# Kernel tuning notes

Hardware: AMD Instinct MI355X
Metric: run time of the kernel (lower is better)

## Reference

```python
import jax, jax.numpy as jnp
import numpy as np

N = 1024       # sentence length (words incl. root at index 0)
WD = 300       # word embedding dim (GloVe-style)
PD = 25        # pos_emb_dim
H = 125        # hidden_dim_lstm
FC = 100       # hidden_dim_fc
PVOCAB = 50    # POS tagset size


def setup_inputs() -> dict:
    key = jax.random.key(0)
    ks = jax.random.split(key, 14)
    f = lambda k, s: jax.random.normal(k, s, dtype=jnp.float32) * 0.1
    d_in = WD + PD
    return {
        "word_vecs": jax.random.normal(ks[0], (N, WD), dtype=jnp.float32),
        "pos_idx": jax.random.randint(ks[1], (N,), 0, PVOCAB),
        "parents_ids": jax.random.randint(ks[2], (N,), 0, N),
        "pos_emb": f(ks[3], (PVOCAB, PD)),
        "Wih0": f(ks[4], (2, 4 * H, d_in)),
        "Whh0": f(ks[5], (2, 4 * H, H)),
        "b0": f(ks[6], (2, 4 * H)),
        "Wih1": f(ks[7], (2, 4 * H, 2 * H)),
        "Whh1": f(ks[8], (2, 4 * H, H)),
        "b1": f(ks[9], (2, 4 * H)),
        "fc1_W": f(ks[10], (FC, 4 * H)),
        "fc1_b": f(ks[11], (FC,)),
        "fc2_W": f(ks[12], (1, FC)),
        "fc2_b": f(ks[13], (1,)),
    }


def _lstm_dir(x, Wih, Whh, b, reverse):
    # torch LSTM cell, gate order (i, f, g, o); b = b_ih + b_hh
    Hd = Whh.shape[1]
    def step(carry, xt):
        h, c = carry
        g = xt @ Wih.T + h @ Whh.T + b
        i, fg, gg, o = jnp.split(g, 4)
        i = jax.nn.sigmoid(i)
        fg = jax.nn.sigmoid(fg)
        gg = jnp.tanh(gg)
        o = jax.nn.sigmoid(o)
        c = fg * c + i * gg
        h = o * jnp.tanh(c)
        return (h, c), h
    init = (jnp.zeros((Hd,), x.dtype), jnp.zeros((Hd,), x.dtype))
    _, hs = jax.lax.scan(step, init, x, reverse=reverse)
    return hs  # [n, H], already in original time order


def _bilstm_layer(x, Wih, Whh, b):
    hf = _lstm_dir(x, Wih[0], Whh[0], b[0], False)
    hb = _lstm_dir(x, Wih[1], Whh[1], b[1], True)
    return jnp.concatenate([hf, hb], axis=1)  # [n, 2H]


def reference(word_vecs, pos_idx, parents_ids, pos_emb, Wih0, Whh0, b0,
              Wih1, Whh1, b1, fc1_W, fc1_b, fc2_W, fc2_b):
    # encoder: concat word + pos embeddings, 2-layer BiLSTM
    x = jnp.concatenate([word_vecs, pos_emb[pos_idx]], axis=1)  # [n, WD+PD]
    h = _bilstm_layer(x, Wih0, Whh0, b0)
    h = _bilstm_layer(h, Wih1, Whh1, b1)  # [n, 2H]
    n = h.shape[0]
    twoH = h.shape[1]
    # fc1(cat(h_i, h_j)) = h_i @ W_head^T + h_j @ W_child^T + b  (vectorized over all pairs)
    A = h @ fc1_W[:, :twoH].T   # head contribution  [n, FC]
    B = h @ fc1_W[:, twoH:].T   # child contribution [n, FC]
    T = jnp.tanh(A[:, None, :] + B[None, :, :] + fc1_b)  # [n, n, FC]
    raw = T @ fc2_W[0] + fc2_b[0]                         # [n, n]
    ii = jnp.arange(n)
    # original loop skips diagonal and arcs into the root (j == 0); those stay 0
    mask = (ii[:, None] != ii[None, :]) & (ii[None, :] != 0)
    scores_mat = jnp.where(mask, raw, jnp.float32(0.0))
    logits = scores_mat.T  # row j = scores of heads for child j
    logp = jax.nn.log_softmax(logits, axis=1)
    loss = -jnp.mean(logp[jnp.arange(n), parents_ids])
    return loss, scores_mat
```

## Files before the change

kernel.cpp:

```cpp
#include <hip/hip_runtime.h>

typedef float v2f __attribute__((ext_vector_type(2)));
typedef float v4f __attribute__((ext_vector_type(4)));

#define LOG2E 1.4426950408889634f
#define LN2   0.6931471805599453f

__device__ __forceinline__ float fexp2(float x) {
  float r; asm("v_exp_f32 %0, %1" : "=v"(r) : "v"(x)); return r;
}
__device__ __forceinline__ float fexp2n(float x) {
  float r; asm("v_exp_f32 %0, -%1" : "=v"(r) : "v"(x)); return r;
}
__device__ __forceinline__ float frcp(float x) {
  float r; asm("v_rcp_f32 %0, %1" : "=v"(r) : "v"(x)); return r;
}
__device__ __forceinline__ float flog2(float x) {
  float r; asm("v_log_f32 %0, %1" : "=v"(r) : "v"(x)); return r;
}
__device__ __forceinline__ void pkfma(v2f& c, v2f a, v2f b) {
  asm("v_pk_fma_f32 %0, %1, %2, %0" : "+v"(c) : "v"(a), "v"(b));
}
__device__ __forceinline__ float dpp_xor1(float v) {
  return __builtin_bit_cast(float,
      __builtin_amdgcn_update_dpp(0, __builtin_bit_cast(int, v), 0xB1, 0xF, 0xF, true));
}
__device__ __forceinline__ float dpp_xor2(float v) {
  return __builtin_bit_cast(float,
      __builtin_amdgcn_update_dpp(0, __builtin_bit_cast(int, v), 0x4E, 0xF, 0xF, true));
}
__device__ __forceinline__ void barrier_lgkm() {
  asm volatile("s_waitcnt lgkmcnt(0)\n\ts_barrier" ::: "memory");
}

__global__ void k_embed(const float* __restrict__ wv, const int* __restrict__ pidx,
                        const float* __restrict__ pemb, float* __restrict__ X) {
  int t = blockIdx.x;
  int pi = pidx[t];
  for (int c = threadIdx.x; c < 336; c += 128) {
    float v;
    if (c < 300)      v = wv[t * 300 + c];
    else if (c < 325) v = pemb[pi * 25 + (c - 300)];
    else              v = 0.f;
    X[t * 336 + c] = v;
  }
}

__global__ void k_repack(const float* __restrict__ src, float* __restrict__ dst,
                         int sK, int dK, int doScale) {
  int r = blockIdx.x;
  float sc = 1.f;
  if (doScale) { int gate = (r % 500) / 125; sc = (gate == 2) ? 0.5f * LOG2E : 0.25f * LOG2E; }
  for (int c = threadIdx.x; c < dK; c += 128)
    dst[r * dK + c] = (c < sK) ? src[r * sK + c] * sc : 0.f;
}

__global__ void k_bscale(const float* __restrict__ b, float* __restrict__ bs) {
  int i = blockIdx.x * 256 + threadIdx.x;
  if (i < 1000) {
    int gate = (i % 500) / 125;
    bs[i] = b[i] * ((gate == 2) ? 0.5f * LOG2E : 0.25f * LOG2E);
  }
}

__global__ void k_wab(const float* __restrict__ fc1W, float* __restrict__ Wab) {
  int r = blockIdx.x;
  int sr = (r < 100) ? r : r - 100;
  int so = (r < 100) ? 0 : 250;
  for (int c = threadIdx.x; c < 256; c += 128)
    Wab[r * 256 + c] = (c < 250) ? fc1W[sr * 500 + so + c] : 0.f;
}

__global__ void k_misc(const float* __restrict__ fc1b, const float* __restrict__ fc2W,
                       float* __restrict__ biasAB, float* __restrict__ sumw) {
  __shared__ float red[128];
  int t = threadIdx.x;
  for (int c = t; c < 256; c += 128)
    biasAB[c] = (c < 100) ? fc1b[c] : 0.f;
  float s = (t < 100) ? fc2W[t] : 0.f;
  red[t] = s; __syncthreads();
  for (int off = 64; off; off >>= 1) {
    if (t < off) red[t] += red[t + off];
    __syncthreads();
  }
  if (t == 0) sumw[0] = red[0];
}

#define BM 64
#define BN 64
#define BKK 16
__global__ __launch_bounds__(256) void k_gemm(
    const float* __restrict__ A, const float* __restrict__ Bw,
    const float* __restrict__ bias, float* __restrict__ C,
    int M, int N, int K, int ldC, long sBz, long sCz, long sbz, int transOut) {
  const int z = blockIdx.z;
  const float* Bp = Bw + (size_t)z * sBz;
  const float* bp = bias + (size_t)z * sbz;
  float* Cp = C + (size_t)z * sCz;
  const int bm = blockIdx.y * BM, bn = blockIdx.x * BN;
  __shared__ __align__(16) float As[BKK][BM + 4];
  __shared__ __align__(16) float Bs[BKK][BN + 4];
  const int tid = threadIdx.x;
  const int tx = tid & 15, ty = tid >> 4;
  const int lr = tid >> 2;
  const int lk = (tid & 3) * 4;
  float acc[4][4];
#pragma unroll
  for (int a = 0; a < 4; ++a)
#pragma unroll
    for (int b = 0; b < 4; ++b) acc[a][b] = 0.f;

  int brow = bn + lr; if (brow >= N) brow = N - 1;
  for (int k0 = 0; k0 < K; k0 += BKK) {
    float4 a4 = *(const float4*)(A + (size_t)(bm + lr) * K + k0 + lk);
    float4 b4 = *(const float4*)(Bp + (size_t)brow * K + k0 + lk);
    __syncthreads();
    As[lk + 0][lr] = a4.x; As[lk + 1][lr] = a4.y; As[lk + 2][lr] = a4.z; As[lk + 3][lr] = a4.w;
    Bs[lk + 0][lr] = b4.x; Bs[lk + 1][lr] = b4.y; Bs[lk + 2][lr] = b4.z; Bs[lk + 3][lr] = b4.w;
    __syncthreads();
#pragma unroll
    for (int kk = 0; kk < BKK; ++kk) {
      float4 av = *(const float4*)&As[kk][ty * 4];
      float4 bv = *(const float4*)&Bs[kk][tx * 4];
      float aa[4] = {av.x, av.y, av.z, av.w};
      float bb[4] = {bv.x, bv.y, bv.z, bv.w};
#pragma unroll
      for (int a = 0; a < 4; ++a)
#pragma unroll
        for (int b = 0; b < 4; ++b)
          acc[a][b] = __builtin_fmaf(aa[a], bb[b], acc[a][b]);
    }
  }
  if (transOut == 0) {
#pragma unroll
    for (int a = 0; a < 4; ++a) {
      int i = bm + ty * 4 + a;
#pragma unroll
      for (int b = 0; b < 4; ++b) {
        int j = bn + tx * 4 + b;
        if (j < N) Cp[(size_t)i * ldC + j] = acc[a][b] + bp[j];
      }
    }
  } else {
#pragma unroll
    for (int a = 0; a < 4; ++a) {
      int i = bm + ty * 4 + a;
#pragma unroll
      for (int b = 0; b < 4; ++b) {
        int j = bn + tx * 4 + b;
        if (j < N) {
          int g = j / 125, u2 = j - g * 125;
          Cp[(size_t)u2 * 4096 + i * 4 + g] = acc[a][b] + bp[j];
        }
      }
    }
  }
}

#define REC_BODY(FWD)                                                              \
  {                                                                                \
    float cst = 0.f;                                                               \
    float4 cur[4], nxt[4];                                                         \
    _Pragma("unroll")                                                              \
    for (int e = 0; e < 4; ++e) cur[e] = Pr4[(FWD ? 0 : 1020) + e];                \
    __syncthreads();                                                               \
    for (int cb = 0; cb < 256; ++cb) {                                             \
      int nc = (cb + 1 < 256) ? cb + 1 : cb;                                       \
      int nb = FWD ? 4 * nc : 1020 - 4 * nc;                                       \
      _Pragma("unroll")                                                            \
      for (int e = 0; e < 4; ++e) nxt[e] = Pr4[nb + e];                            \
      _Pragma("unroll")                                                            \
      for (int e = 0; e < 4; ++e) {                                                \
        const int buf = e & 1;                                                     \
        float4 pre = cur[FWD ? e : 3 - e];                                         \
        const v4f* hp = (const v4f*)&hb[buf][36 * sub];                            \
        v2f a0 = {0.f, 0.f}, a1 = {0.f, 0.f}, a2 = {0.f, 0.f}, a3 = {0.f, 0.f};    \
        _Pragma("unroll")                                                          \
        for (int q = 0; q < 4; ++q) {                                              \
          v4f h1v = hp[2 * q], h2v = hp[2 * q + 1];                                \
          v2f ha = __builtin_shufflevector(h1v, h1v, 0, 1);                        \
          v2f hc = __builtin_shufflevector(h1v, h1v, 2, 3);                        \
          v2f he = __builtin_shufflevector(h2v, h2v, 0, 1);                        \
          v2f hg = __builtin_shufflevector(h2v, h2v, 2, 3);                        \
          pkfma(a0, w0[4 * q], ha); pkfma(a0, w0[4 * q + 1], hc);                  \
          pkfma(a0, w0[4 * q + 2], he); pkfma(a0, w0[4 * q + 3], hg);              \
          pkfma(a1, w1[4 * q], ha); pkfma(a1, w1[4 * q + 1], hc);                  \
          pkfma(a1, w1[4 * q + 2], he); pkfma(a1, w1[4 * q + 3], hg);              \
          pkfma(a2, w2[4 * q], ha); pkfma(a2, w2[4 * q + 1], hc);                  \
          pkfma(a2, w2[4 * q + 2], he); pkfma(a2, w2[4 * q + 3], hg);              \
          pkfma(a3, w3[4 * q], ha); pkfma(a3, w3[4 * q + 1], hc);                  \
          pkfma(a3, w3[4 * q + 2], he); pkfma(a3, w3[4 * q + 3], hg);              \
        }                                                                          \
        float p0 = a0.x + a0.y + pre.x;                                            \
        float p1 = a1.x + a1.y + pre.y;                                            \
        float p2 = a2.x + a2.y + pre.z;                                            \
        float p3 = a3.x + a3.y + pre.w;                                            \
        p0 += dpp_xor1(p0); p0 += dpp_xor2(p0);                                    \
        p1 += dpp_xor1(p1); p1 += dpp_xor2(p1);                                    \
        p2 += dpp_xor1(p2); p2 += dpp_xor2(p2);                                    \
        p3 += dpp_xor1(p3); p3 += dpp_xor2(p3);                                    \
        float gi = frcp(1.f + fexp2n(p0));                                         \
        float gf = frcp(1.f + fexp2n(p1));                                         \
        float gg = __builtin_fmaf(2.f, frcp(1.f + fexp2n(p2)), -1.f);              \
        float go = frcp(1.f + fexp2n(p3));                                         \
        cst = __builtin_fmaf(gf, cst, gi * gg);                                    \
        float th = __builtin_fmaf(2.f, frcp(1.f + fexp2n(cst * (2.f * LOG2E))), -1.f); \
        float h = go * th;                                                         \
        if (wr) {                                                                  \
          hb[buf ^ 1][u + 4 * (u >> 5)] = h;                                       \
          int step = 4 * cb + e;                                                   \
          int time = FWD ? step : 1023 - step;                                     \
          hout[(size_t)time * 256 + d * 125 + u] = h;                              \
        }                                                                          \
        barrier_lgkm();                                                            \
      }                                                                            \
      cur[0] = nxt[0]; cur[1] = nxt[1]; cur[2] = nxt[2]; cur[3] = nxt[3];          \
    }                                                                              \
  }

__global__ __launch_bounds__(512, 2) void k_rec(const float* __restrict__ Pq,
                                                const float* __restrict__ Whh,
                                                float* __restrict__ hout) {
  const int d = blockIdx.x;
  const int t = threadIdx.x;
  int u = t >> 2; if (u > 124) u = 124;
  const int sub = t & 3;
  const bool wr = (sub == 0) && ((t >> 2) < 125);

  const float* Wd = Whh + (size_t)d * 500 * 125;
  v2f w0[16], w1[16], w2[16], w3[16];
#pragma unroll
  for (int j = 0; j < 16; ++j) {
    int col = sub * 32 + 2 * j;
    const float* r0 = Wd + (size_t)(0 * 125 + u) * 125;
    const float* r1 = Wd + (size_t)(1 * 125 + u) * 125;
    const float* r2 = Wd + (size_t)(2 * 125 + u) * 125;
    const float* r3 = Wd + (size_t)(3 * 125 + u) * 125;
    bool c0 = col < 125, c1 = col + 1 < 125;
    v2f a, b, c, dd;
    a.x  = c0 ? r0[col] * LOG2E : 0.f;          a.y  = c1 ? r0[col + 1] * LOG2E : 0.f;
    b.x  = c0 ? r1[col] * LOG2E : 0.f;          b.y  = c1 ? r1[col + 1] * LOG2E : 0.f;
    c.x  = c0 ? r2[col] * 2.f * LOG2E : 0.f;    c.y  = c1 ? r2[col + 1] * 2.f * LOG2E : 0.f;
    dd.x = c0 ? r3[col] * LOG2E : 0.f;          dd.y = c1 ? r3[col + 1] * LOG2E : 0.f;
    w0[j] = a; w1[j] = b; w2[j] = c; w3[j] = dd;
  }

  __shared__ __align__(16) float hb[2][160];
  for (int i = t; i < 320; i += 512) ((float*)hb)[i] = 0.f;

  const float4* Pr4 = (const float4*)(Pq + (size_t)d * 500 * 1024) + (size_t)u * 1024;

  if (d == 0) REC_BODY(1)
  else        REC_BODY(0)
}

__global__ __launch_bounds__(256) void k_pair(const float* __restrict__ AB,
    const float* __restrict__ fc2W, const float* __restrict__ fc2b,
    const float* __restrict__ sumw, float* __restrict__ outS,
    float* __restrict__ scoresT) {
  __shared__ float As[32][100];
  __shared__ float Bs[32][101];
  __shared__ float w2s[100];
  const int tid = threadIdx.x;
  const int i0 = blockIdx.y * 32, j0 = blockIdx.x * 32;
  for (int idx = tid; idx < 3200; idx += 256) {
    int r = idx / 100, k = idx - r * 100;
    As[r][k] = AB[(size_t)(i0 + r) * 200 + k];
    Bs[r][k] = AB[(size_t)(j0 + r) * 200 + 100 + k];
  }
  if (tid < 100) w2s[tid] = 2.f * fc2W[tid];
  __syncthreads();
  const int tx = tid & 31, ty = tid >> 5;
  float acc[4] = {0.f, 0.f, 0.f, 0.f};
#pragma unroll 4
  for (int k = 0; k < 100; ++k) {
    float b = Bs[tx][k];
    float wk2 = w2s[k];
    float bs = b * (2.f * LOG2E);
#pragma unroll
    for (int q = 0; q < 4; ++q) {
      float a = As[ty + 8 * q][k];
      float r = frcp(1.f + fexp2(__builtin_fmaf(a, 2.f * LOG2E, bs)));
      acc[q] = __builtin_fmaf(wk2, r, acc[q]);
    }
  }
  float base = sumw[0] + fc2b[0];
  const int j = j0 + tx;
#pragma unroll
  for (int q = 0; q < 4; ++q) {
    int i = i0 + ty + 8 * q;
    float val = (i != j && j != 0) ? (base - acc[q]) : 0.f;
    outS[(size_t)i * 1024 + j] = val;
    scoresT[(size_t)j * 1024 + i] = val;
  }
}

__global__ __launch_bounds__(256) void k_soft(const float* __restrict__ scoresT,
    const int* __restrict__ parents, float* __restrict__ contrib) {
  const int j = blockIdx.x, tid = threadIdx.x;
  __shared__ float red[256];
  const float* row = scoresT + (size_t)j * 1024;
  float v0 = row[tid], v1 = row[tid + 256], v2 = row[tid + 512], v3 = row[tid + 768];
  float m = fmaxf(fmaxf(v0, v1), fmaxf(v2, v3));
  red[tid] = m; __syncthreads();
  for (int off = 128; off; off >>= 1) {
    if (tid < off) red[tid] = fmaxf(red[tid], red[tid + off]);
    __syncthreads();
  }
  m = red[0]; __syncthreads();
  float s = fexp2((v0 - m) * LOG2E) + fexp2((v1 - m) * LOG2E) +
            fexp2((v2 - m) * LOG2E) + fexp2((v3 - m) * LOG2E);
  red[tid] = s; __syncthreads();
  for (int off = 128; off; off >>= 1) {
    if (tid < off) red[tid] += red[tid + off];
    __syncthreads();
  }
  if (tid == 0) {
    float S = red[0];
    int p = parents[j];
    contrib[j] = row[p] - m - flog2(S) * LN2;
  }
}

__global__ __launch_bounds__(256) void k_loss(const float* __restrict__ contrib,
                                              float* __restrict__ out) {
  __shared__ float red[256];
  int tid = threadIdx.x;
  float s = contrib[tid] + contrib[tid + 256] + contrib[tid + 512] + contrib[tid + 768];
  red[tid] = s; __syncthreads();
  for (int off = 128; off; off >>= 1) {
    if (tid < off) red[tid] += red[tid + off];
    __syncthreads();
  }
  if (tid == 0) out[0] = -red[0] * (1.f / 1024.f);
}

extern "C" void kernel_launch(void* const* d_in, const int* in_sizes, int n_in,
                              void* d_out, int out_size, void* d_ws, size_t ws_size,
                              hipStream_t stream) {
  const float* wv   = (const float*)d_in[0];
  const int*   pidx = (const int*)d_in[1];
  const int*   par  = (const int*)d_in[2];
  const float* pemb = (const float*)d_in[3];
  const float* Wih0 = (const float*)d_in[4];
  const float* Whh0 = (const float*)d_in[5];
  const float* b0   = (const float*)d_in[6];
  const float* Wih1 = (const float*)d_in[7];
  const float* Whh1 = (const float*)d_in[8];
  const float* b1   = (const float*)d_in[9];
  const float* fc1W = (const float*)d_in[10];
  const float* fc1b = (const float*)d_in[11];
  const float* fc2W = (const float*)d_in[12];
  const float* fc2b = (const float*)d_in[13];
  float* ws = (float*)d_ws;
  float* X      = ws + 0;
  float* Wih0p  = ws + 344064;
  float* Pq0    = ws + 680064;
  float* h0     = ws + 1704064;
  float* Wih1p  = ws + 1966208;
  float* Pq1    = ws + 2222208;
  float* h1     = ws + 3246208;
  float* Wab    = ws + 3508352;
  float* biasAB = ws + 3559552;
  float* AB     = ws + 3559808;
  float* scT    = ws + 3764608;
  float* contrib= ws + 4813184;
  float* sumw   = ws + 4814208;
  float* bs0    = ws + 4814212;
  float* bs1    = ws + 4815212;
  float* out = (float*)d_out;

  hipMemsetAsync(h0, 0, 1024 * 256 * sizeof(float), stream);
  hipMemsetAsync(h1, 0, 1024 * 256 * sizeof(float), stream);

  k_embed <<<1024, 128, 0, stream>>>(wv, pidx, pemb, X);
  k_repack<<<1000, 128, 0, stream>>>(Wih0, Wih0p, 325, 336, 1);
  k_repack<<<1000, 128, 0, stream>>>(Wih1, Wih1p, 250, 256, 1);
  k_bscale<<<4, 256, 0, stream>>>(b0, bs0);
  k_bscale<<<4, 256, 0, stream>>>(b1, bs1);
  k_wab   <<<200, 128, 0, stream>>>(fc1W, Wab);
  k_misc  <<<1, 128, 0, stream>>>(fc1b, fc2W, biasAB, sumw);

  k_gemm<<<dim3(8, 16, 2), 256, 0, stream>>>(X, Wih0p, bs0, Pq0, 1024, 500, 336, 0,
                                             500L * 336, 500L * 1024, 500L, 2);
  k_rec <<<2, 512, 0, stream>>>(Pq0, Whh0, h0);
  k_gemm<<<dim3(8, 16, 2), 256, 0, stream>>>(h0, Wih1p, bs1, Pq1, 1024, 500, 256, 0,
                                             500L * 256, 500L * 1024, 500L, 2);
  k_rec <<<2, 512, 0, stream>>>(Pq1, Whh1, h1);
  k_gemm<<<dim3(4, 16, 1), 256, 0, stream>>>(h1, Wab, biasAB, AB, 1024, 200, 256, 200,
                                             0L, 0L, 0L, 0);
  k_pair<<<dim3(32, 32), 256, 0, stream>>>(AB, fc2W, fc2b, sumw, out + 1, scT);
  k_soft<<<1024, 256, 0, stream>>>(scT, par, contrib);
  k_loss<<<1, 256, 0, stream>>>(contrib, out);
}
```

Baseline: 1.368 ms.

## Fuse prep kernels, fold tanh scale into cell state, launch redundant recurrence blocks

Merges the seven small preprocessing kernels into one block-dispatched k_prep launch to cut launch overhead. It rescales the g-gate so the cell state is kept pre-multiplied by 2*log2e, which removes one multiply from the serial recurrence chain. The recurrence is now launched with 128 blocks instead of 2. Only the first two blocks write output, while the other 126 redo the same work, apparently to keep clocks or power state high, at the cost of wasted compute and possible contention.

New measurement: 1.394 ms. No clear change (+1.8%).

```diff
diff --git a/kernel.cpp b/kernel.cpp
--- a/kernel.cpp
+++ b/kernel.cpp
@@ -33,57 +33,68 @@
   asm volatile("s_waitcnt lgkmcnt(0)\n\ts_barrier" ::: "memory");
 }
 
-__global__ void k_embed(const float* __restrict__ wv, const int* __restrict__ pidx,
-                        const float* __restrict__ pemb, float* __restrict__ X) {
-  int t = blockIdx.x;
-  int pi = pidx[t];
-  for (int c = threadIdx.x; c < 336; c += 128) {
-    float v;
-    if (c < 300)      v = wv[t * 300 + c];
-    else if (c < 325) v = pemb[pi * 25 + (c - 300)];
-    else              v = 0.f;
-    X[t * 336 + c] = v;
-  }
-}
-
-__global__ void k_repack(const float* __restrict__ src, float* __restrict__ dst,
-                         int sK, int dK, int doScale) {
-  int r = blockIdx.x;
-  float sc = 1.f;
-  if (doScale) { int gate = (r % 500) / 125; sc = (gate == 2) ? 0.5f * LOG2E : 0.25f * LOG2E; }
-  for (int c = threadIdx.x; c < dK; c += 128)
-    dst[r * dK + c] = (c < sK) ? src[r * sK + c] * sc : 0.f;
-}
-
-__global__ void k_bscale(const float* __restrict__ b, float* __restrict__ bs) {
-  int i = blockIdx.x * 256 + threadIdx.x;
-  if (i < 1000) {
-    int gate = (i % 500) / 125;
-    bs[i] = b[i] * ((gate == 2) ? 0.5f * LOG2E : 0.25f * LOG2E);
-  }
-}
-
-__global__ void k_wab(const float* __restrict__ fc1W, float* __restrict__ Wab) {
-  int r = blockIdx.x;
-  int sr = (r < 100) ? r : r - 100;
-  int so = (r < 100) ? 0 : 250;
-  for (int c = threadIdx.x; c < 256; c += 128)
-    Wab[r * 256 + c] = (c < 250) ? fc1W[sr * 500 + so + c] : 0.f;
-}
-
-__global__ void k_misc(const float* __restrict__ fc1b, const float* __restrict__ fc2W,
-                       float* __restrict__ biasAB, float* __restrict__ sumw) {
-  __shared__ float red[128];
-  int t = threadIdx.x;
-  for (int c = t; c < 256; c += 128)
-    biasAB[c] = (c < 100) ? fc1b[c] : 0.f;
-  float s = (t < 100) ? fc2W[t] : 0.f;
-  red[t] = s; __syncthreads();
-  for (int off = 64; off; off >>= 1) {
-    if (t < off) red[t] += red[t + off];
-    __syncthreads();
-  }
-  if (t == 0) sumw[0] = red[0];
+__global__ __launch_bounds__(128) void k_prep(
+    const float* __restrict__ wv, const int* __restrict__ pidx,
+    const float* __restrict__ pemb, float* __restrict__ X,
+    const float* __restrict__ Wih0, float* __restrict__ Wih0p,
+    const float* __restrict__ Wih1, float* __restrict__ Wih1p,
+    const float* __restrict__ fc1W, float* __restrict__ Wab,
+    const float* __restrict__ fc1b, const float* __restrict__ fc2W,
+    float* __restrict__ biasAB, float* __restrict__ sumw,
+    const float* __restrict__ b0, float* __restrict__ bs0,
+    const float* __restrict__ b1, float* __restrict__ bs1) {
+  const int b = blockIdx.x, tid = threadIdx.x;
+  if (b < 1024) {
+    int t = b, pi = pidx[t];
+    for (int c = tid; c < 336; c += 128) {
+      float v;
+      if (c < 300)      v = wv[t * 300 + c];
+      else if (c < 325) v = pemb[pi * 25 + (c - 300)];
+      else              v = 0.f;
+      X[t * 336 + c] = v;
+    }
+  } else if (b < 2024) {
+    int r = b - 1024;
+    int gate = (r % 500) / 125;
+    float sc = (gate == 2) ? 0.5f * LOG2E : 0.25f * LOG2E;
+    for (int c = tid; c < 336; c += 128)
+      Wih0p[r * 336 + c] = (c < 325) ? Wih0[r * 325 + c] * sc : 0.f;
+  } else if (b < 3024) {
+    int r = b - 2024;
+    int gate = (r % 500) / 125;
+    float sc = (gate == 2) ? 0.5f * LOG2E : 0.25f * LOG2E;
+    for (int c = tid; c < 256; c += 128)
+      Wih1p[r * 256 + c] = (c < 250) ? Wih1[r * 250 + c] * sc : 0.f;
+  } else if (b < 3224) {
+    int r = b - 3024;
+    int sr = (r < 100) ? r : r - 100;
+    int so = (r < 100) ? 0 : 250;
+    for (int c = tid; c < 256; c += 128)
+      Wab[r * 256 + c] = (c < 250) ? fc1W[sr * 500 + so + c] : 0.f;
+  } else if (b == 3224) {
+    __shared__ float red[128];
+    for (int c = tid; c < 256; c += 128)
+      biasAB[c] = (c < 100) ? fc1b[c] : 0.f;
+    float s = (tid < 100) ? fc2W[tid] : 0.f;
+    red[tid] = s; __syncthreads();
+    for (int off = 64; off; off >>= 1) {
+      if (tid < off) red[tid] += red[tid + off];
+      __syncthreads();
+    }
+    if (tid == 0) sumw[0] = red[0];
+  } else if (b < 3233) {
+    int i = (b - 3225) * 128 + tid;
+    if (i < 1000) {
+      int gate = (i % 500) / 125;
+      bs0[i] = b0[i] * ((gate == 2) ? 0.5f * LOG2E : 0.25f * LOG2E);
+    }
+  } else {
+    int i = (b - 3233) * 128 + tid;
+    if (i < 1000) {
+      int gate = (i % 500) / 125;
+      bs1[i] = b1[i] * ((gate == 2) ? 0.5f * LOG2E : 0.25f * LOG2E);
+    }
+  }
 }
 
 #define BM 64
@@ -201,16 +212,20 @@
         p3 += dpp_xor1(p3); p3 += dpp_xor2(p3);                                    \
         float gi = frcp(1.f + fexp2n(p0));                                         \
         float gf = frcp(1.f + fexp2n(p1));                                         \
-        float gg = __builtin_fmaf(2.f, frcp(1.f + fexp2n(p2)), -1.f);              \
+                             \
+        float gg2 = __builtin_fmaf(4.f * LOG2E, frcp(1.f + fexp2n(p2)),            \
+                                   -2.f * LOG2E);                                  \
         float go = frcp(1.f + fexp2n(p3));                                         \
-        cst = __builtin_fmaf(gf, cst, gi * gg);                                    \
-        float th = __builtin_fmaf(2.f, frcp(1.f + fexp2n(cst * (2.f * LOG2E))), -1.f); \
+        cst = __builtin_fmaf(gf, cst, gi * gg2);          \
+        float th = __builtin_fmaf(2.f, frcp(1.f + fexp2n(cst)), -1.f);             \
         float h = go * th;                                                         \
         if (wr) {                                                                  \
           hb[buf ^ 1][u + 4 * (u >> 5)] = h;                                       \
           int step = 4 * cb + e;                                                   \
           int time = FWD ? step : 1023 - step;                                     \
           hout[(size_t)time * 256 + d * 125 + u] = h;                              \
+        } else if (sub == 0) {                                                     \
+          hb[buf ^ 1][u + 4 * (u >> 5)] = h;                                       \
         }                                                                          \
         barrier_lgkm();                                                            \
       }                                                                            \
@@ -221,11 +236,11 @@
 __global__ __launch_bounds__(512, 2) void k_rec(const float* __restrict__ Pq,
                                                 const float* __restrict__ Whh,
                                                 float* __restrict__ hout) {
-  const int d = blockIdx.x;
+  const int d = blockIdx.x & 1;
   const int t = threadIdx.x;
   int u = t >> 2; if (u > 124) u = 124;
   const int sub = t & 3;
-  const bool wr = (sub == 0) && ((t >> 2) < 125);
+  const bool wr = (sub == 0) && ((t >> 2) < 125) && (blockIdx.x < 2);
 
   const float* Wd = Whh + (size_t)d * 500 * 125;
   v2f w0[16], w1[16], w2[16], w3[16];
@@ -373,20 +388,16 @@
   hipMemsetAsync(h0, 0, 1024 * 256 * sizeof(float), stream);
   hipMemsetAsync(h1, 0, 1024 * 256 * sizeof(float), stream);
 
-  k_embed <<<1024, 128, 0, stream>>>(wv, pidx, pemb, X);
-  k_repack<<<1000, 128, 0, stream>>>(Wih0, Wih0p, 325, 336, 1);
-  k_repack<<<1000, 128, 0, stream>>>(Wih1, Wih1p, 250, 256, 1);
-  k_bscale<<<4, 256, 0, stream>>>(b0, bs0);
-  k_bscale<<<4, 256, 0, stream>>>(b1, bs1);
-  k_wab   <<<200, 128, 0, stream>>>(fc1W, Wab);
-  k_misc  <<<1, 128, 0, stream>>>(fc1b, fc2W, biasAB, sumw);
+  k_prep<<<3241, 128, 0, stream>>>(wv, pidx, pemb, X, Wih0, Wih0p, Wih1, Wih1p,
+                                   fc1W, Wab, fc1b, fc2W, biasAB, sumw,
+                                   b0, bs0, b1, bs1);
 
   k_gemm<<<dim3(8, 16, 2), 256, 0, stream>>>(X, Wih0p, bs0, Pq0, 1024, 500, 336, 0,
                                              500L * 336, 500L * 1024, 500L, 2);
-  k_rec <<<2, 512, 0, stream>>>(Pq0, Whh0, h0);
+  k_rec <<<128, 512, 0, stream>>>(Pq0, Whh0, h0);
   k_gemm<<<dim3(8, 16, 2), 256, 0, stream>>>(h0, Wih1p, bs1, Pq1, 1024, 500, 256, 0,
                                              500L * 256, 500L * 1024, 500L, 2);
-  k_rec <<<2, 512, 0, stream>>>(Pq1, Whh1, h1);
+  k_rec <<<128, 512, 0, stream>>>(Pq1, Whh1, h1);
   k_gemm<<<dim3(4, 16, 1), 256, 0, stream>>>(h1, Wab, biasAB, AB, 1024, 200, 256, 200,
                                              0L, 0L, 0L, 0);
   k_pair<<<dim3(32, 32), 256, 0, stream>>>(AB, fc2W, fc2b, sumw, out + 1, scT);
```
